# Optimization experiments

Hardware: AMD Instinct MI355X
Metric: run time of the kernel (lower is better)

Reference implementation:

```python
import jax, jax.numpy as jnp
import numpy as np

B, S, HID, H = 4, 2048, 1024, 16
D = HID // H  # dim per head


def setup_inputs() -> dict:
    key = jax.random.key(0)
    ks = jax.random.split(key, 7)
    inp = {
        "q": jax.random.normal(ks[0], (B, S, HID), dtype=jnp.float32),
        "k": jax.random.normal(ks[1], (B, S, HID), dtype=jnp.float32),
        "v": jax.random.normal(ks[2], (B, S, HID), dtype=jnp.float32),
        # Linear weights stored as (in, out); applied as x @ W. use_bias=False.
        "Wq": jax.random.normal(ks[3], (HID, HID), dtype=jnp.float32) * (1.0 / np.sqrt(HID)),
        "Wk": jax.random.normal(ks[4], (HID, HID), dtype=jnp.float32) * (1.0 / np.sqrt(HID)),
        "Wv": jax.random.normal(ks[5], (HID, HID), dtype=jnp.float32) * (1.0 / np.sqrt(HID)),
        "Wo": jax.random.normal(ks[6], (HID, HID), dtype=jnp.float32) * (1.0 / np.sqrt(HID)),
    }
    return inp


def reference(q, k, v, Wq, Wk, Wv, Wo):
    scale = 1.0 / jnp.sqrt(jnp.float32(D))
    # QKV projections, then split hidden into (H, D) heads (same layout as transpose_qkv)
    Q = (q @ Wq).reshape(B, S, H, D)
    K = (k @ Wk).reshape(B, S, H, D)
    V = (v @ Wv).reshape(B, S, H, D)
    # scaled dot-product attention: full [B,H,S,S] score matrix, softmax over keys
    attn_w = jnp.einsum("bqhd,bkhd->bhqk", Q, K) * scale
    attn_w = jax.nn.softmax(attn_w, axis=-1)
    # dropout rate is 0 (eval-mode / deterministic)
    O = jnp.einsum("bhqk,bkhd->bqhd", attn_w, V).reshape(B, S, HID)
    return O @ Wo
```

## Files before the change

### kernel.cpp

```cpp
#include <hip/hip_runtime.h>


typedef __attribute__((ext_vector_type(8))) short short8;
typedef __attribute__((ext_vector_type(4))) float float4v;
typedef __attribute__((ext_vector_type(16))) float float16v;
typedef __attribute__((ext_vector_type(2))) unsigned int uint2v;

#if __has_builtin(__builtin_amdgcn_exp2f)
#define EXP2F(x) __builtin_amdgcn_exp2f(x)
#else
#define EXP2F(x) exp2f(x)
#endif

__device__ __forceinline__ unsigned short f2b(float x) {
  return (unsigned short)((__float_as_uint(x) + 0x8000u) >> 16);
}
__device__ __forceinline__ unsigned pk2f(float a, float b) {
  unsigned ua = __float_as_uint(a) + 0x8000u;
  unsigned ub = __float_as_uint(b) + 0x8000u;
  return __builtin_amdgcn_perm(ub, ua, 0x07060302);
}
__device__ __forceinline__ unsigned cvtpk(float a, float b) {
  unsigned r;
  asm("v_cvt_pk_bf16_f32 %0, %1, %2" : "=v"(r) : "v"(a), "v"(b));
  return r;
}

typedef __attribute__((address_space(3))) unsigned int lds_uint;
typedef const __attribute__((address_space(1))) unsigned int gbl_uint;
__device__ __forceinline__ void stage16(const unsigned short* g, unsigned short* l) {
#if __has_builtin(__builtin_amdgcn_global_load_lds)
  __builtin_amdgcn_global_load_lds((gbl_uint*)g, (lds_uint*)l, 16, 0, 0);
#else
  *(uint4*)l = *(const uint4*)g;
#endif
}

__global__ __launch_bounds__(256) void conv_qkv(const float* __restrict__ q,
                                                const float* __restrict__ k,
                                                const float* __restrict__ v,
                                                unsigned short* __restrict__ ws,
                                                float qscale) {
  const int z = blockIdx.y;
  const float* src = z == 0 ? q : (z == 1 ? k : v);
  unsigned short* dst = ws + (size_t)z * 8388608;
  const float s = z == 0 ? qscale : 1.0f;
  size_t i = ((size_t)blockIdx.x * 256 + threadIdx.x) * 8;
  float4v a = *(const float4v*)(src + i);
  float4v b = *(const float4v*)(src + i + 4);
  uint4 o;
  o.x = pk2f(a.x * s, a.y * s);
  o.y = pk2f(a.z * s, a.w * s);
  o.z = pk2f(b.x * s, b.y * s);
  o.w = pk2f(b.z * s, b.w * s);
  *(uint4*)(dst + i) = o;
}

__global__ __launch_bounds__(256) void wtrans(const float* __restrict__ Wq,
                                              const float* __restrict__ Wk,
                                              const float* __restrict__ Wv,
                                              const float* __restrict__ Wo,
                                              unsigned short* __restrict__ Wt) {
  __shared__ float tile[32][33];
  const float* W = blockIdx.z == 0 ? Wq : blockIdx.z == 1 ? Wk
                   : blockIdx.z == 2 ? Wv : Wo;
  unsigned short* T = Wt + (size_t)blockIdx.z * 1048576;
  const int tx = threadIdx.x & 31, ty = threadIdx.x >> 5;
  const int k0 = blockIdx.y * 32, n0 = blockIdx.x * 32;
#pragma unroll
  for (int i = 0; i < 4; i++)
    tile[ty + 8 * i][tx] = W[(size_t)(k0 + ty + 8 * i) * 1024 + n0 + tx];
  __syncthreads();
#pragma unroll
  for (int i = 0; i < 4; i++)
    T[(size_t)(n0 + ty + 8 * i) * 1024 + k0 + tx] = f2b(tile[tx][ty + 8 * i]);
}

template <int MODE, bool SWAP>
__global__ __launch_bounds__(256, 2) void gemm_bt(const unsigned short* __restrict__ A,
                                                  const unsigned short* __restrict__ Bt,
                                                  void* __restrict__ Cg) {
  __shared__ __align__(16) unsigned short As[2][128 * 64];
  __shared__ __align__(16) unsigned short Bs[2][128 * 64];
  const int tid = threadIdx.x;
  const int lane = tid & 63;
  const int w = tid >> 6;
  const int quad = lane >> 4, col = lane & 15;
  const int wm = w >> 1, wn = w & 1;
  const int lin = blockIdx.x;
  const int xcd = lin & 7, grp = lin >> 3;
  const int m0 = ((grp & 7) * 8 + xcd) * 128;
  const int n0 = (grp >> 3) * 128;
  const int rA = lane >> 3, cA = lane & 7;

  float4v acc[4][4] = {};

  auto STAGE = [&](int b, int k0) {
#pragma unroll
    for (int j = 0; j < 4; j++) {
      const int row = w * 32 + j * 8 + rA;
      stage16(A + (unsigned)(m0 + row) * 1024 + k0 + ((cA ^ rA) * 8),
              &As[b][row * 64 + cA * 8]);
      stage16(Bt + (unsigned)(n0 + row) * 1024 + k0 + ((cA ^ rA) * 8),
              &Bs[b][row * 64 + cA * 8]);
    }
  };

  STAGE(0, 0);
  __syncthreads();

  int cur = 0;
  for (int k0 = 0; k0 < 1024; k0 += 64) {
    if (k0 < 960) STAGE(cur ^ 1, k0 + 64);

#pragma unroll
    for (int ks = 0; ks < 2; ks++) {
      short8 af[4], bf[4];
#pragma unroll
      for (int mi = 0; mi < 4; mi++) {
        int row = wm * 64 + mi * 16 + col;
        af[mi] = *(const short8*)&As[cur][row * 64 + (((ks * 4 + quad) ^ (col & 7)) * 8)];
      }
#pragma unroll
      for (int ni = 0; ni < 4; ni++) {
        int row = wn * 64 + ni * 16 + col;
        bf[ni] = *(const short8*)&Bs[cur][row * 64 + (((ks * 4 + quad) ^ (col & 7)) * 8)];
      }
#pragma unroll
      for (int mi = 0; mi < 4; mi++)
#pragma unroll
        for (int ni = 0; ni < 4; ni++) {
          if (SWAP)
            acc[ni][mi] = __builtin_amdgcn_mfma_f32_16x16x32_bf16(
                bf[ni], af[mi], acc[ni][mi], 0, 0, 0);
          else
            acc[mi][ni] = __builtin_amdgcn_mfma_f32_16x16x32_bf16(
                af[mi], bf[ni], acc[mi][ni], 0, 0, 0);
        }
    }

    __syncthreads();
    cur ^= 1;
  }

  if (MODE == 0) {
#pragma unroll
    for (int ni = 0; ni < 4; ni++) {
      const int cg = n0 + wn * 64 + ni * 16 + quad * 4;
      const int h = cg >> 6, dlo = cg & 63;
#pragma unroll
      for (int mi = 0; mi < 4; mi++) {
        const int tok = m0 + wm * 64 + mi * 16 + col;
        const int b = tok >> 11, s = tok & 2047;
        uint2 pk;
        pk.x = pk2f(acc[ni][mi][0], acc[ni][mi][1]);
        pk.y = pk2f(acc[ni][mi][2], acc[ni][mi][3]);
        *(uint2*)((unsigned short*)Cg +
                  ((unsigned)((b * 16 + h) * 2048 + s) * 64 + dlo)) = pk;
      }
    }
  } else if (MODE == 1) {
#pragma unroll
    for (int mi = 0; mi < 4; mi++) {
      const int tok = m0 + wm * 64 + mi * 16 + quad * 4;
      const int b = tok >> 11, s = tok & 2047;
#pragma unroll
      for (int ni = 0; ni < 4; ni++) {
        const int cg = n0 + wn * 64 + ni * 16 + col;
        const int h = cg >> 6, d = cg & 63;
        uint2 pk;
        pk.x = pk2f(acc[mi][ni][0], acc[mi][ni][1]);
        pk.y = pk2f(acc[mi][ni][2], acc[mi][ni][3]);
        *(uint2*)((unsigned short*)Cg +
                  ((unsigned)((b * 16 + h) * 64 + d) * 2048 + s)) = pk;
      }
    }
  } else {
#pragma unroll
    for (int mi = 0; mi < 4; mi++) {
      const int row = m0 + wm * 64 + mi * 16 + quad * 4;
#pragma unroll
      for (int ni = 0; ni < 4; ni++) {
        const int cg = n0 + wn * 64 + ni * 16 + col;
#pragma unroll
        for (int r = 0; r < 4; r++)
          ((float*)Cg)[(unsigned)(row + r) * 1024 + cg] = acc[mi][ni][r];
      }
    }
  }
}

__global__ __launch_bounds__(256, 4) void attn_kernel(
    const unsigned short* __restrict__ Qb, const unsigned short* __restrict__ Kb,
    const unsigned short* __restrict__ Vt, unsigned short* __restrict__ Ob) {
  __shared__ __align__(16) unsigned short K_lds[2][64 * 64];
  __shared__ __align__(16) unsigned short V_lds[2][64 * 64];

  const int tid = threadIdx.x;
  const int lane = tid & 63;
  const int w = tid >> 6;
  const int l5 = lane & 31, hi = lane >> 5;

  const int lin = blockIdx.x;
  const int bh = ((lin >> 3) & 7) * 8 + (lin & 7);
  const int qt = lin >> 6;

  const unsigned short* Kbase = Kb + (size_t)bh * (2048 * 64);
  const unsigned short* Vbase = Vt + (size_t)bh * (64 * 2048);
  const int q0 = qt * 128 + w * 32;

  short8 qf[4];
#pragma unroll
  for (int c = 0; c < 4; c++)
    qf[c] = *(const short8*)(Qb + ((size_t)bh * 2048 + q0 + l5) * 64 + c * 16 + hi * 8);

  short8 onef;
#pragma unroll
  for (int j = 0; j < 8; j++) onef[j] = (short)0x3F80;

  float16v oacc[2] = {};
  float16v dacc = {};

  const int sr = lane >> 3, sc = lane & 7;

  auto STAGE = [&](int b, int kt) {
    const int s0 = kt * 64;
#pragma unroll
    for (int j = 0; j < 2; j++) {
      const int row = w * 16 + j * 8 + sr;
      stage16(Kbase + (unsigned)(s0 + row) * 64 + ((sc ^ sr) * 8),
              &K_lds[b][row * 64 + sc * 8]);
      stage16(Vbase + (unsigned)row * 2048 + s0 + ((sc ^ sr) * 8),
              &V_lds[b][row * 64 + sc * 8]);
    }
  };

  STAGE(0, 0);
  __syncthreads();

  int cur = 0;
  for (int kt = 0; kt < 32; kt++) {
    if (kt < 31) STAGE(cur ^ 1, kt + 1);

    const unsigned short* Kl = &K_lds[cur][0];
    const unsigned short* Vl = &V_lds[cur][0];

    short8 pf[4];
#pragma unroll
    for (int t = 0; t < 2; t++) {
      float16v sacc = {};
      __builtin_amdgcn_s_setprio(1);
#pragma unroll
      for (int c = 0; c < 4; c++) {
        short8 kf = *(const short8*)&Kl[(t * 32 + l5) * 64 +
                                        (((c * 2 + hi) ^ (l5 & 7)) * 8)];
        sacc = __builtin_amdgcn_mfma_f32_32x32x16_bf16(kf, qf[c], sacc, 0, 0, 0);
      }
      __builtin_amdgcn_s_setprio(0);

#pragma unroll
      for (int half = 0; half < 2; half++) {
        const int k0 = half * 8;
        unsigned P0 = cvtpk(EXP2F(sacc[k0 + 0]), EXP2F(sacc[k0 + 1]));
        unsigned P1 = cvtpk(EXP2F(sacc[k0 + 2]), EXP2F(sacc[k0 + 3]));
        unsigned P2 = cvtpk(EXP2F(sacc[k0 + 4]), EXP2F(sacc[k0 + 5]));
        unsigned P3 = cvtpk(EXP2F(sacc[k0 + 6]), EXP2F(sacc[k0 + 7]));
        unsigned u0, u1, u2, u3;
#if __has_builtin(__builtin_amdgcn_permlane32_swap)
        uint2v a02 = __builtin_amdgcn_permlane32_swap(P0, P2, false, false);
        uint2v a13 = __builtin_amdgcn_permlane32_swap(P1, P3, false, false);
        u0 = a02[0]; u2 = a02[1];
        u1 = a13[0]; u3 = a13[1];
#else
        unsigned p0s = __shfl_xor((int)P0, 32), p2s = __shfl_xor((int)P2, 32);
        unsigned p1s = __shfl_xor((int)P1, 32), p3s = __shfl_xor((int)P3, 32);
        u0 = hi ? p2s : P0; u2 = hi ? P2 : p0s;
        u1 = hi ? p3s : P1; u3 = hi ? P3 : p1s;
#endif
        union { unsigned u[4]; short8 s; } cv;
        cv.u[0] = u0; cv.u[1] = u1; cv.u[2] = u2; cv.u[3] = u3;
        pf[t * 2 + half] = cv.s;
      }
    }

    __builtin_amdgcn_s_setprio(1);
#pragma unroll
    for (int dt = 0; dt < 2; dt++)
#pragma unroll
      for (int kc = 0; kc < 4; kc++) {
        short8 vf = *(const short8*)&Vl[(dt * 32 + l5) * 64 +
                                        (((kc * 2 + hi) ^ (l5 & 7)) * 8)];
        oacc[dt] = __builtin_amdgcn_mfma_f32_32x32x16_bf16(vf, pf[kc], oacc[dt], 0, 0, 0);
      }
#pragma unroll
    for (int kc = 0; kc < 4; kc++)
      dacc = __builtin_amdgcn_mfma_f32_32x32x16_bf16(onef, pf[kc], dacc, 0, 0, 0);
    __builtin_amdgcn_s_setprio(0);

    __syncthreads();
    cur ^= 1;
  }

  const float rd = 1.f / dacc[0];

  const int b = bh >> 4, h = bh & 15;
  const unsigned obase = (unsigned)(b * 2048 + q0 + l5) * 1024 + h * 64;
#pragma unroll
  for (int dt = 0; dt < 2; dt++)
#pragma unroll
    for (int g = 0; g < 4; g++) {
      uint2 pk;
      pk.x = cvtpk(oacc[dt][4 * g + 0] * rd, oacc[dt][4 * g + 1] * rd);
      pk.y = cvtpk(oacc[dt][4 * g + 2] * rd, oacc[dt][4 * g + 3] * rd);
      *(uint2*)(Ob + obase + dt * 32 + 8 * g + 4 * hi) = pk;
    }
}

extern "C" void kernel_launch(void* const* d_in, const int* in_sizes, int n_in,
                              void* d_out, int out_size, void* d_ws, size_t ws_size,
                              hipStream_t stream) {
  const float* q = (const float*)d_in[0];
  const float* k = (const float*)d_in[1];
  const float* v = (const float*)d_in[2];
  const float* Wq = (const float*)d_in[3];
  const float* Wk = (const float*)d_in[4];
  const float* Wv = (const float*)d_in[5];
  const float* Wo = (const float*)d_in[6];

  unsigned short* ws = (unsigned short*)d_ws;
  unsigned short* qb = ws;
  unsigned short* kb = ws + 8388608;
  unsigned short* vb = ws + 16777216;
  unsigned short* Qb = ws + 25165824;
  unsigned short* Kb = ws + 33554432;
  unsigned short* Vt = ws + 41943040;
  unsigned short* Wt = ws + 50331648;

  dim3 blk(256);
  const float qscale = 0.18033688011112042f;

  conv_qkv<<<dim3(4096, 3), blk, 0, stream>>>(q, k, v, ws, qscale);
  wtrans<<<dim3(32, 32, 4), blk, 0, stream>>>(Wq, Wk, Wv, Wo, Wt);

  gemm_bt<0, true><<<dim3(512), blk, 0, stream>>>(qb, Wt + 0 * 1048576, Qb);
  gemm_bt<0, true><<<dim3(512), blk, 0, stream>>>(kb, Wt + 1 * 1048576, Kb);
  gemm_bt<1, false><<<dim3(512), blk, 0, stream>>>(vb, Wt + 2 * 1048576, Vt);

  attn_kernel<<<dim3(1024), blk, 0, stream>>>(Qb, Kb, Vt, qb );

  gemm_bt<2, false><<<dim3(512), blk, 0, stream>>>(qb , Wt + 3 * 1048576,
                                                   (float*)d_out);
}
```

Before: 339.4 us.

## Merge QKV projection GEMMs into one launch with K=32 tiles and higher occupancy

The three separate Q/K/V projection GEMM launches become a single 1536-block launch that dispatches on block index. The GEMM K-tile shrinks from 64 to 32 with a new XOR swizzle, which halves LDS per block so launch bounds can rise from 2 to 4 blocks per SM. This cuts launch overhead and tail effects and adds latency hiding through occupancy, at the cost of twice as many K-loop iterations and barriers.

```diff
diff --git a/kernel.cpp b/kernel.cpp
--- a/kernel.cpp
+++ b/kernel.cpp
@@ -77,32 +77,33 @@
 }
 
 template <int MODE, bool SWAP>
-__global__ __launch_bounds__(256, 2) void gemm_bt(const unsigned short* __restrict__ A,
-                                                  const unsigned short* __restrict__ Bt,
-                                                  void* __restrict__ Cg) {
-  __shared__ __align__(16) unsigned short As[2][128 * 64];
-  __shared__ __align__(16) unsigned short Bs[2][128 * 64];
+__device__ __forceinline__ void gemm_core(const unsigned short* __restrict__ A,
+                                          const unsigned short* __restrict__ Bt,
+                                          void* __restrict__ Cg, int lin,
+                                          unsigned short (*__restrict__ As)[128 * 32],
+                                          unsigned short (*__restrict__ Bs)[128 * 32]) {
   const int tid = threadIdx.x;
   const int lane = tid & 63;
   const int w = tid >> 6;
   const int quad = lane >> 4, col = lane & 15;
   const int wm = w >> 1, wn = w & 1;
-  const int lin = blockIdx.x;
   const int xcd = lin & 7, grp = lin >> 3;
   const int m0 = ((grp & 7) * 8 + xcd) * 128;
   const int n0 = (grp >> 3) * 128;
-  const int rA = lane >> 3, cA = lane & 7;
+
+  const int srow = tid >> 2, schunk = tid & 3;
+  const int sg = schunk ^ (srow & 3) ^ ((srow >> 2) & 3);
 
   float4v acc[4][4] = {};
 
   auto STAGE = [&](int b, int k0) {
 #pragma unroll
-    for (int j = 0; j < 4; j++) {
-      const int row = w * 32 + j * 8 + rA;
-      stage16(A + (unsigned)(m0 + row) * 1024 + k0 + ((cA ^ rA) * 8),
-              &As[b][row * 64 + cA * 8]);
-      stage16(Bt + (unsigned)(n0 + row) * 1024 + k0 + ((cA ^ rA) * 8),
-              &Bs[b][row * 64 + cA * 8]);
+    for (int j = 0; j < 2; j++) {
+      const int row = j * 64 + srow;
+      stage16(A + (unsigned)(m0 + row) * 1024 + k0 + sg * 8,
+              &As[b][row * 32 + schunk * 8]);
+      stage16(Bt + (unsigned)(n0 + row) * 1024 + k0 + sg * 8,
+              &Bs[b][row * 32 + schunk * 8]);
     }
   };
 
@@ -110,34 +111,33 @@
   __syncthreads();
 
   int cur = 0;
-  for (int k0 = 0; k0 < 1024; k0 += 64) {
-    if (k0 < 960) STAGE(cur ^ 1, k0 + 64);
-
-#pragma unroll
-    for (int ks = 0; ks < 2; ks++) {
-      short8 af[4], bf[4];
-#pragma unroll
-      for (int mi = 0; mi < 4; mi++) {
-        int row = wm * 64 + mi * 16 + col;
-        af[mi] = *(const short8*)&As[cur][row * 64 + (((ks * 4 + quad) ^ (col & 7)) * 8)];
-      }
+  for (int k0 = 0; k0 < 1024; k0 += 32) {
+    if (k0 < 992) STAGE(cur ^ 1, k0 + 32);
+
+    short8 af[4], bf[4];
+#pragma unroll
+    for (int mi = 0; mi < 4; mi++) {
+      const int row = wm * 64 + mi * 16 + col;
+      af[mi] = *(const short8*)&As[cur][row * 32 +
+                                        ((quad ^ (row & 3) ^ ((row >> 2) & 3)) * 8)];
+    }
+#pragma unroll
+    for (int ni = 0; ni < 4; ni++) {
+      const int row = wn * 64 + ni * 16 + col;
+      bf[ni] = *(const short8*)&Bs[cur][row * 32 +
+                                        ((quad ^ (row & 3) ^ ((row >> 2) & 3)) * 8)];
+    }
+#pragma unroll
+    for (int mi = 0; mi < 4; mi++)
 #pragma unroll
       for (int ni = 0; ni < 4; ni++) {
-        int row = wn * 64 + ni * 16 + col;
-        bf[ni] = *(const short8*)&Bs[cur][row * 64 + (((ks * 4 + quad) ^ (col & 7)) * 8)];
-      }
-#pragma unroll
-      for (int mi = 0; mi < 4; mi++)
-#pragma unroll
-        for (int ni = 0; ni < 4; ni++) {
-          if (SWAP)
-            acc[ni][mi] = __builtin_amdgcn_mfma_f32_16x16x32_bf16(
-                bf[ni], af[mi], acc[ni][mi], 0, 0, 0);
-          else
-            acc[mi][ni] = __builtin_amdgcn_mfma_f32_16x16x32_bf16(
-                af[mi], bf[ni], acc[mi][ni], 0, 0, 0);
-        }
-    }
+        if (SWAP)
+          acc[ni][mi] = __builtin_amdgcn_mfma_f32_16x16x32_bf16(
+              bf[ni], af[mi], acc[ni][mi], 0, 0, 0);
+        else
+          acc[mi][ni] = __builtin_amdgcn_mfma_f32_16x16x32_bf16(
+              af[mi], bf[ni], acc[mi][ni], 0, 0, 0);
+      }
 
     __syncthreads();
     cur ^= 1;
@@ -188,6 +188,29 @@
       }
     }
   }
+}
+
+__global__ __launch_bounds__(256, 4) void gemm_qkv(const unsigned short* __restrict__ act,
+                                                   const unsigned short* __restrict__ Wt,
+                                                   unsigned short* __restrict__ out) {
+  __shared__ __align__(16) unsigned short As[2][128 * 32];
+  __shared__ __align__(16) unsigned short Bs[2][128 * 32];
+  const int z = blockIdx.x >> 9, r = blockIdx.x & 511;
+  if (z < 2)
+    gemm_core<0, true>(act + (size_t)z * 8388608, Wt + (size_t)z * 1048576,
+                       out + (size_t)z * 8388608, r, As, Bs);
+  else
+    gemm_core<1, false>(act + (size_t)2 * 8388608, Wt + (size_t)2 * 1048576,
+                        out + (size_t)2 * 8388608, r, As, Bs);
+}
+
+template <int MODE, bool SWAP>
+__global__ __launch_bounds__(256, 4) void gemm_bt(const unsigned short* __restrict__ A,
+                                                  const unsigned short* __restrict__ Bt,
+                                                  void* __restrict__ Cg) {
+  __shared__ __align__(16) unsigned short As[2][128 * 32];
+  __shared__ __align__(16) unsigned short Bs[2][128 * 32];
+  gemm_core<MODE, SWAP>(A, Bt, Cg, blockIdx.x, As, Bs);
 }
 
 __global__ __launch_bounds__(256, 4) void attn_kernel(
@@ -329,8 +352,6 @@
 
   unsigned short* ws = (unsigned short*)d_ws;
   unsigned short* qb = ws;
-  unsigned short* kb = ws + 8388608;
-  unsigned short* vb = ws + 16777216;
   unsigned short* Qb = ws + 25165824;
   unsigned short* Kb = ws + 33554432;
   unsigned short* Vt = ws + 41943040;
@@ -342,9 +363,7 @@
   conv_qkv<<<dim3(4096, 3), blk, 0, stream>>>(q, k, v, ws, qscale);
   wtrans<<<dim3(32, 32, 4), blk, 0, stream>>>(Wq, Wk, Wv, Wo, Wt);
 
-  gemm_bt<0, true><<<dim3(512), blk, 0, stream>>>(qb, Wt + 0 * 1048576, Qb);
-  gemm_bt<0, true><<<dim3(512), blk, 0, stream>>>(kb, Wt + 1 * 1048576, Kb);
-  gemm_bt<1, false><<<dim3(512), blk, 0, stream>>>(vb, Wt + 2 * 1048576, Vt);
+  gemm_qkv<<<dim3(1536), blk, 0, stream>>>(ws, Wt, Qb);
 
   attn_kernel<<<dim3(1024), blk, 0, stream>>>(Qb, Kb, Vt, qb );
 
```

After: 323.1 us. -4.8%, faster.
